# Optimization experiments

Hardware: AMD Instinct MI355X
Metric: run time of the kernel (lower is better)

Reference implementation:

```python
import jax, jax.numpy as jnp
import numpy as np

L, D, F, H = 4, 1024, 2048, 8
DH = D // H
EPS = 1e-5


def setup_inputs() -> dict:
    key = jax.random.key(0)
    ks = jax.random.split(key, 8)
    B, S = 4, 1024
    sd = 1.0 / np.sqrt(D)
    sf = 1.0 / np.sqrt(F)
    return {
        "X": jax.random.normal(ks[0], (B, S, D), jnp.float32),
        "Wq": jax.random.normal(ks[1], (L, D, D), jnp.float32) * sd,
        "Wk": jax.random.normal(ks[2], (L, D, D), jnp.float32) * sd,
        "Wv": jax.random.normal(ks[3], (L, D, D), jnp.float32) * sd,
        "Wg": jax.random.normal(ks[4], (L, D, D), jnp.float32) * sd,
        "Wo": jax.random.normal(ks[5], (L, D, D), jnp.float32) * sd,
        "W1": jax.random.normal(ks[6], (L, D, F), jnp.float32) * sd,
        "W2": jax.random.normal(ks[7], (L, F, D), jnp.float32) * sf,
        "ln_scale": jnp.ones((D,), jnp.float32),
        "ln_bias": jnp.zeros((D,), jnp.float32),
        "gn_scale": jnp.ones((L, D), jnp.float32),
        "gn_bias": jnp.zeros((L, D), jnp.float32),
    }


def _layer_norm(x, scale, bias):
    mu = x.mean(-1, keepdims=True)
    var = x.var(-1, keepdims=True)
    return (x - mu) * jax.lax.rsqrt(var + EPS) * scale + bias


def _rotate(x, cos, sin):
    # x: (B,S,H,DH); cos/sin: (1,S,1,DH//2); rotary pairs (even, odd)
    x1, x2 = x[..., 0::2], x[..., 1::2]
    r1 = x1 * cos - x2 * sin
    r2 = x1 * sin + x2 * cos
    return jnp.stack([r1, r2], axis=-1).reshape(x.shape)


def _decay_matrix(S):
    # D[h,n,m] = gamma_h^(n-m) for n>=m else 0
    gammas = 1.0 - jnp.exp(jnp.linspace(np.log(1 / 32), np.log(1 / 512), H)).astype(jnp.float32)
    n = jnp.arange(S)
    diff = (n[:, None] - n[None, :]).astype(jnp.float32)
    pw = jnp.exp(jnp.clip(diff, 0.0)[None] * jnp.log(gammas)[:, None, None])
    return jnp.where(diff[None] >= 0, pw, 0.0)  # (H,S,S)


def _retention(x, Wq, Wk, Wv, Wg, Wo, gn_s, gn_b, Dm, cos, sin):
    B, S, _ = x.shape
    Q = (x @ Wq).reshape(B, S, H, DH)
    K = (x @ Wk).reshape(B, S, H, DH)
    V = (x @ Wv).reshape(B, S, H, DH)
    Q = _rotate(Q, cos, sin)
    K = _rotate(K, cos, -sin)  # conjugate phase
    att = jnp.einsum('bnhd,bmhd->bhnm', Q, K) * Dm  # (B,H,S,S)
    Y = jnp.einsum('bhnm,bmhd->bnhd', att, V)
    # group norm: normalize each head's output per token
    mu = Y.mean(-1, keepdims=True)
    var = Y.var(-1, keepdims=True)
    Y = (Y - mu) * jax.lax.rsqrt(var + EPS)
    Y = Y.reshape(B, S, D) * gn_s + gn_b
    G = jax.nn.swish(x @ Wg)
    return (G * Y) @ Wo


def reference(X, Wq, Wk, Wv, Wg, Wo, W1, W2, ln_scale, ln_bias, gn_scale, gn_bias):
    B, S, _ = X.shape
    pos = jnp.arange(S, dtype=jnp.float32)
    inv_freq = 1.0 / (10000.0 ** (jnp.arange(0, DH, 2, dtype=jnp.float32) / DH))
    ang = pos[:, None] * inv_freq[None, :]  # (S, DH//2)
    cos = jnp.cos(ang)[None, :, None, :]
    sin = jnp.sin(ang)[None, :, None, :]
    Dm = _decay_matrix(S)
    for i in range(L):
        Yr = _retention(_layer_norm(X, ln_scale, ln_bias), Wq[i], Wk[i], Wv[i],
                        Wg[i], Wo[i], gn_scale[i], gn_bias[i], Dm, cos, sin) + X
        X = jax.nn.gelu(_layer_norm(Yr, ln_scale, ln_bias) @ W1[i]) @ W2[i] + Yr
    return X
```

## Files before the change

### kernel.cpp

```cpp
#include <hip/hip_runtime.h>
#include <hip/hip_bf16.h>
#include <cmath>

#define LAYERS 4
#define Bb 4
#define Ss 1024
#define Dd 1024
#define Ff 2048
#define Hh 8
#define DHd 128
#define Mm (Bb * Ss)
#define EPSf 1e-5f
#define LDQ 4096

typedef __attribute__((ext_vector_type(8))) short short8v;
typedef __attribute__((ext_vector_type(4))) float f32x4;
typedef __attribute__((ext_vector_type(4))) unsigned int u32x4;

__device__ __forceinline__ float swish_f(float x) { return x / (1.f + expf(-x)); }
__device__ __forceinline__ float gelu_f(float x) {
  return 0.5f * x * (1.f + tanhf(0.7978845608028654f * (x + 0.044715f * x * x * x)));
}
__device__ __forceinline__ unsigned short f2bfu(float f) {
  __hip_bfloat16 h = __float2bfloat16(f);
  return __builtin_bit_cast(unsigned short, h);
}
__device__ __forceinline__ float bfu2f(unsigned short u) {
  unsigned v = ((unsigned)u) << 16;
  return __builtin_bit_cast(float, v);
}
__device__ __forceinline__ void gl_lds16(const void* g, void* l) {
  __builtin_amdgcn_global_load_lds((__attribute__((address_space(1))) void*)g,
                                   (__attribute__((address_space(3))) void*)l, 16, 0, 0);
}
__device__ __forceinline__ f32x4 mfma16(short8v a, short8v b, f32x4 c) {
  return __builtin_amdgcn_mfma_f32_16x16x32_bf16(a, b, c, 0, 0, 0);
}

__global__ __launch_bounds__(256) void ln_bf16_kernel(const float* __restrict__ x,
                                                      short* __restrict__ outb,
                                                      const float* __restrict__ sc,
                                                      const float* __restrict__ bi) {
  const int row = blockIdx.x;
  const int t = threadIdx.x;
  const float4 v = *(const float4*)(x + (size_t)row * Dd + t * 4);
  float s = v.x + v.y + v.z + v.w;
  float s2 = v.x * v.x + v.y * v.y + v.z * v.z + v.w * v.w;
#pragma unroll
  for (int o = 32; o > 0; o >>= 1) { s += __shfl_down(s, o); s2 += __shfl_down(s2, o); }
  __shared__ float ps[4], ps2[4];
  if ((t & 63) == 0) { ps[t >> 6] = s; ps2[t >> 6] = s2; }
  __syncthreads();
  s = ps[0] + ps[1] + ps[2] + ps[3];
  s2 = ps2[0] + ps2[1] + ps2[2] + ps2[3];
  const float mu = s * (1.f / Dd);
  const float var = s2 * (1.f / Dd) - mu * mu;
  const float rstd = rsqrtf(var + EPSf);
  const float4 g = *(const float4*)(sc + t * 4);
  const float4 b = *(const float4*)(bi + t * 4);
  const float o0 = (v.x - mu) * rstd * g.x + b.x;
  const float o1 = (v.y - mu) * rstd * g.y + b.y;
  const float o2 = (v.z - mu) * rstd * g.z + b.z;
  const float o3 = (v.w - mu) * rstd * g.w + b.w;
  unsigned p0 = (unsigned)f2bfu(o0) | ((unsigned)f2bfu(o1) << 16);
  unsigned p1 = (unsigned)f2bfu(o2) | ((unsigned)f2bfu(o3) << 16);
  uint2 pk; pk.x = p0; pk.y = p1;
  *(uint2*)(outb + (size_t)row * Dd + t * 4) = pk;
}

__global__ void rope_table_kernel(float* __restrict__ ct, float* __restrict__ st) {
  const int i = blockIdx.x * 256 + threadIdx.x;
  const int s = i >> 6, f = i & 63;
  const float inv = powf(10000.f, -(float)f / 64.f);
  const float a = (float)s * inv;
  ct[i] = cosf(a);
  st[i] = sinf(a);
}

__global__ void rope_ip_kernel(short* __restrict__ QK, const float* __restrict__ ct,
                               const float* __restrict__ st) {
  const int idx = blockIdx.x * 256 + threadIdx.x;
  const int f = idx & 63;
  const int h = (idx >> 6) & 7;
  const int r = idx >> 9;
  const int s = r & (Ss - 1);
  const float c = ct[(s << 6) + f], sn = st[(s << 6) + f];
  const size_t qo = (size_t)r * LDQ + h * DHd + 2 * f;
  const unsigned qp = *(const unsigned*)(QK + qo);
  const unsigned kp = *(const unsigned*)(QK + qo + 1024);
  const float qx = bfu2f((unsigned short)(qp & 0xffff)), qy = bfu2f((unsigned short)(qp >> 16));
  const float kx = bfu2f((unsigned short)(kp & 0xffff)), ky = bfu2f((unsigned short)(kp >> 16));
  const unsigned qn = (unsigned)f2bfu(qx * c - qy * sn) | ((unsigned)f2bfu(qx * sn + qy * c) << 16);
  const unsigned kn = (unsigned)f2bfu(kx * c + ky * sn) | ((unsigned)f2bfu(-kx * sn + ky * c) << 16);
  *(unsigned*)(QK + qo) = qn;
  *(unsigned*)(QK + qo + 1024) = kn;
}

__global__ __launch_bounds__(256) void wtrans4_kernel(const float* __restrict__ W0,
                                                      const float* __restrict__ W1,
                                                      const float* __restrict__ W2,
                                                      const float* __restrict__ W3,
                                                      short* __restrict__ Wt) {
  __shared__ float tile[32][33];
  const int t = threadIdx.x;
  const int n0 = blockIdx.x * 32, k0 = blockIdx.y * 32;
  const int which = n0 >> 10;
  const float* W = (which == 0) ? W0 : (which == 1) ? W1 : (which == 2) ? W2 : W3;
  const int nl = n0 & 1023;
  const int tc = t & 31, tr8 = t >> 5;
#pragma unroll
  for (int i = 0; i < 4; ++i) {
    const int r = tr8 + i * 8;
    tile[r][tc] = W[(size_t)(k0 + r) * 1024 + nl + tc];
  }
  __syncthreads();
#pragma unroll
  for (int i = 0; i < 4; ++i) {
    const int r = tr8 + i * 8;
    Wt[(size_t)(n0 + r) * 1024 + k0 + tc] = (short)f2bfu(tile[tc][r]);
  }
}

__global__ __launch_bounds__(256) void wtrans1_kernel(const float* __restrict__ W,
                                                      short* __restrict__ Wt, int K, int N) {
  __shared__ float tile[32][33];
  const int t = threadIdx.x;
  const int n0 = blockIdx.x * 32, k0 = blockIdx.y * 32;
  const int tc = t & 31, tr8 = t >> 5;
#pragma unroll
  for (int i = 0; i < 4; ++i) {
    const int r = tr8 + i * 8;
    tile[r][tc] = W[(size_t)(k0 + r) * N + n0 + tc];
  }
  __syncthreads();
#pragma unroll
  for (int i = 0; i < 4; ++i) {
    const int r = tr8 + i * 8;
    Wt[(size_t)(n0 + r) * K + k0 + tc] = (short)f2bfu(tile[tc][r]);
  }
}

__global__ __launch_bounds__(256) void vtrans16_kernel(const short* __restrict__ Vb,
                                                       short* __restrict__ Vt) {
  __shared__ short tile[32][33];
  const int t = threadIdx.x;
  const int s0 = blockIdx.x * 32, d0 = blockIdx.y * 32, bh = blockIdx.z;
  const int bb = bh >> 3, h = bh & 7;
  const int tc = t & 31, tr8 = t >> 5;
#pragma unroll
  for (int i = 0; i < 4; ++i) {
    const int r = tr8 + i * 8;
    tile[r][tc] = Vb[(size_t)(bb * Ss + s0 + r) * LDQ + 2048 + h * DHd + d0 + tc];
  }
  __syncthreads();
#pragma unroll
  for (int i = 0; i < 4; ++i) {
    const int r = tr8 + i * 8;
    Vt[(size_t)(bh * DHd + d0 + r) * Ss + s0 + tc] = tile[tc][r];
  }
}

template <int EPI>
__global__ __launch_bounds__(512, 2) void gemm10(const short* __restrict__ A,
                                                 const short* __restrict__ Bt,
                                                 float* __restrict__ Cf,
                                                 short* __restrict__ Cb,
                                                 const float* __restrict__ Res,
                                                 int N, int K, int ldc) {
  __shared__ __align__(16) short As[2][2][128 * 64];
  __shared__ __align__(16) short Bs[2][2][128 * 64];
  const int t = threadIdx.x;
  const int w = t >> 6, l = t & 63;
  const int lq = l >> 4, lr = l & 15;
  const int wr = w >> 2, wc = w & 3;
  const int bhalf = wc >> 1, brow0 = (wc & 1) * 64;
  const int nwg = gridDim.x * gridDim.y;
  const int bid0 = blockIdx.x + blockIdx.y * gridDim.x;
  const int lgid = (bid0 & 7) * (nwg >> 3) + (bid0 >> 3);
  const int bx = lgid % gridDim.x, by = lgid / gridDim.x;
  const int row0 = by * 256, col0 = bx * 256;
  const int NT = K >> 6;

  f32x4 acc[8][4] = {};
  short8v a[4][2], b[4][2];

  auto stageA = [&](int kt, int hf) {
    const int db = kt & 1;
#pragma unroll
    for (int i = 0; i < 2; ++i) {
      const int c = t + i * 512;
      const int row = c >> 3, slot = c & 7;
      gl_lds16(A + (size_t)(row0 + hf * 128 + row) * K + kt * 64 + ((slot ^ (row & 7)) << 3),
               &As[db][hf][c * 8]);
    }
  };
  auto stageB = [&](int kt, int hf) {
    const int db = kt & 1;
#pragma unroll
    for (int i = 0; i < 2; ++i) {
      const int c = t + i * 512;
      const int row = c >> 3, slot = c & 7;
      gl_lds16(Bt + (size_t)(col0 + hf * 128 + row) * K + kt * 64 + ((slot ^ (row & 7)) << 3),
               &Bs[db][hf][c * 8]);
    }
  };
  auto rdA = [&](int db, int m, int ks) -> short8v {
    const int row = m * 16 + lr;
    return *(const short8v*)&As[db][wr][row * 64 + (((ks << 2) + lq) ^ (row & 7)) * 8];
  };
  auto rdB = [&](int db, int n, int ks) -> short8v {
    const int row = brow0 + n * 16 + lr;
    return *(const short8v*)&Bs[db][bhalf][row * 64 + (((ks << 2) + lq) ^ (row & 7)) * 8];
  };

  stageA(0, 0); stageA(0, 1); stageB(0, 0); stageB(0, 1);
  if (NT > 1) { stageB(1, 0); stageB(1, 1); }
  if (NT > 1) { asm volatile("s_waitcnt vmcnt(4)" ::: "memory"); }
  else        { asm volatile("s_waitcnt vmcnt(0)" ::: "memory"); }
  asm volatile("s_barrier" ::: "memory");

  for (int kt = 0; kt < NT; ++kt) {
    const int db = kt & 1;
#pragma unroll
    for (int m = 0; m < 4; ++m) { a[m][0] = rdA(db, m, 0); a[m][1] = rdA(db, m, 1); }
#pragma unroll
    for (int n = 0; n < 2; ++n) { b[n][0] = rdB(db, n, 0); b[n][1] = rdB(db, n, 1); }
    if (kt + 1 < NT) stageA(kt + 1, 0);
    __builtin_amdgcn_s_setprio(1);
#pragma unroll
    for (int m = 0; m < 4; ++m)
#pragma unroll
      for (int n = 0; n < 2; ++n) {
        acc[m][n] = mfma16(a[m][0], b[n][0], acc[m][n]);
        acc[m][n] = mfma16(a[m][1], b[n][1], acc[m][n]);
      }
    __builtin_amdgcn_s_setprio(0);
    asm volatile("s_barrier" ::: "memory");
#pragma unroll
    for (int n = 2; n < 4; ++n) { b[n][0] = rdB(db, n, 0); b[n][1] = rdB(db, n, 1); }
    if (kt + 1 < NT) stageA(kt + 1, 1);
    __builtin_amdgcn_s_setprio(1);
#pragma unroll
    for (int m = 0; m < 4; ++m)
#pragma unroll
      for (int n = 2; n < 4; ++n) {
        acc[m][n] = mfma16(a[m][0], b[n][0], acc[m][n]);
        acc[m][n] = mfma16(a[m][1], b[n][1], acc[m][n]);
      }
    __builtin_amdgcn_s_setprio(0);
    asm volatile("s_barrier" ::: "memory");
#pragma unroll
    for (int m = 0; m < 4; ++m) { a[m][0] = rdA(db, m + 4, 0); a[m][1] = rdA(db, m + 4, 1); }
    if (kt + 2 < NT) stageB(kt + 2, 0);
    __builtin_amdgcn_s_setprio(1);
#pragma unroll
    for (int m = 0; m < 4; ++m)
#pragma unroll
      for (int n = 0; n < 2; ++n) {
        acc[m + 4][n] = mfma16(a[m][0], b[n][0], acc[m + 4][n]);
        acc[m + 4][n] = mfma16(a[m][1], b[n][1], acc[m + 4][n]);
      }
    __builtin_amdgcn_s_setprio(0);
    asm volatile("s_barrier" ::: "memory");
    if (kt + 2 < NT) stageB(kt + 2, 1);
    __builtin_amdgcn_s_setprio(1);
#pragma unroll
    for (int m = 0; m < 4; ++m)
#pragma unroll
      for (int n = 2; n < 4; ++n) {
        acc[m + 4][n] = mfma16(a[m][0], b[n][0], acc[m + 4][n]);
        acc[m + 4][n] = mfma16(a[m][1], b[n][1], acc[m + 4][n]);
      }
    __builtin_amdgcn_s_setprio(0);
    if (kt + 2 < NT) { asm volatile("s_waitcnt vmcnt(4)" ::: "memory"); }
    else             { asm volatile("s_waitcnt vmcnt(0)" ::: "memory"); }
    asm volatile("s_barrier" ::: "memory");
  }

#pragma unroll
  for (int m = 0; m < 8; ++m) {
#pragma unroll
    for (int n = 0; n < 4; ++n) {
#pragma unroll
      for (int r = 0; r < 4; ++r) {
        const int row = row0 + wr * 128 + m * 16 + lq * 4 + r;
        const int col = col0 + wc * 64 + n * 16 + lr;
        const size_t o = (size_t)row * ldc + col;
        float v = acc[m][n][r];
        if (EPI == 0) Cb[o] = (short)f2bfu(v);
        else if (EPI == 1) Cf[o] = v + Res[o];
        else Cb[o] = (short)f2bfu(gelu_f(v));
      }
    }
  }
}

template <int EPI>
__global__ __launch_bounds__(512) void gemm11(const short* __restrict__ A,
                                              const short* __restrict__ Bt,
                                              float* __restrict__ Cf,
                                              short* __restrict__ Cb,
                                              const float* __restrict__ Res,
                                              int K, int lda, int ldb, int ldc, int nxt) {
  __shared__ __align__(16) short As[3][256 * 64];
  __shared__ __align__(16) short Bs[3][128 * 64];
  const int t = threadIdx.x;
  const int w = t >> 6, l = t & 63;
  const int lq = l >> 4, lr = l & 15;
  const int wr = w >> 2, wc = w & 3;
  const int nwg = gridDim.x;
  const int lgid = (blockIdx.x & 7) * (nwg >> 3) + (blockIdx.x >> 3);
  const int mt = lgid / nxt, nt_ = lgid % nxt;
  const int row0 = mt * 256, col0 = nt_ * 128;
  const int NT = K >> 6;
  f32x4 acc[8][2] = {};
  short8v a[4][2], b[2][2];

  auto stageA = [&](int kt, int hf) {
    const int s = kt % 3;
#pragma unroll
    for (int i = 0; i < 2; ++i) {
      const int c = t + i * 512;
      const int row = c >> 3, slot = c & 7;
      gl_lds16(A + (size_t)(row0 + hf * 128 + row) * lda + kt * 64 + ((slot ^ (row & 7)) << 3),
               &As[s][hf * 8192 + c * 8]);
    }
  };
  auto stageB = [&](int kt) {
    const int s = kt % 3;
#pragma unroll
    for (int i = 0; i < 2; ++i) {
      const int c = t + i * 512;
      const int row = c >> 3, slot = c & 7;
      gl_lds16(Bt + (size_t)(col0 + row) * ldb + kt * 64 + ((slot ^ (row & 7)) << 3),
               &Bs[s][c * 8]);
    }
  };
  auto rdA = [&](int s, int m, int ks) -> short8v {
    const int row = wr * 128 + m * 16 + lr;
    return *(const short8v*)&As[s][row * 64 + (((ks << 2) + lq) ^ (row & 7)) * 8];
  };
  auto rdB = [&](int s, int n, int ks) -> short8v {
    const int row = wc * 32 + n * 16 + lr;
    return *(const short8v*)&Bs[s][row * 64 + (((ks << 2) + lq) ^ (row & 7)) * 8];
  };

  stageA(0, 0); stageA(0, 1); stageB(0);
  stageA(1, 0); stageA(1, 1); stageB(1);
  asm volatile("s_waitcnt vmcnt(6)" ::: "memory");
  asm volatile("s_barrier" ::: "memory");

  for (int kt = 0; kt < NT; ++kt) {
    const int s = kt % 3;
#pragma unroll
    for (int m = 0; m < 4; ++m) { a[m][0] = rdA(s, m, 0); a[m][1] = rdA(s, m, 1); }
#pragma unroll
    for (int n = 0; n < 2; ++n) { b[n][0] = rdB(s, n, 0); b[n][1] = rdB(s, n, 1); }
    if (kt + 2 < NT) stageA(kt + 2, 0);
    __builtin_amdgcn_s_setprio(1);
#pragma unroll
    for (int m = 0; m < 4; ++m)
#pragma unroll
      for (int n = 0; n < 2; ++n) {
        acc[m][n] = mfma16(a[m][0], b[n][0], acc[m][n]);
        acc[m][n] = mfma16(a[m][1], b[n][1], acc[m][n]);
      }
    __builtin_amdgcn_s_setprio(0);
    asm volatile("s_barrier" ::: "memory");
#pragma unroll
    for (int m = 0; m < 4; ++m) { a[m][0] = rdA(s, m + 4, 0); a[m][1] = rdA(s, m + 4, 1); }
    if (kt + 2 < NT) { stageA(kt + 2, 1); stageB(kt + 2); }
    __builtin_amdgcn_s_setprio(1);
#pragma unroll
    for (int m = 0; m < 4; ++m)
#pragma unroll
      for (int n = 0; n < 2; ++n) {
        acc[m + 4][n] = mfma16(a[m][0], b[n][0], acc[m + 4][n]);
        acc[m + 4][n] = mfma16(a[m][1], b[n][1], acc[m + 4][n]);
      }
    __builtin_amdgcn_s_setprio(0);
    if (kt + 2 < NT) { asm volatile("s_waitcnt vmcnt(6)" ::: "memory"); }
    else             { asm volatile("s_waitcnt vmcnt(0)" ::: "memory"); }
    asm volatile("s_barrier" ::: "memory");
  }

#pragma unroll
  for (int m = 0; m < 8; ++m) {
#pragma unroll
    for (int n = 0; n < 2; ++n) {
#pragma unroll
      for (int r = 0; r < 4; ++r) {
        const int row = row0 + wr * 128 + m * 16 + lq * 4 + r;
        const int col = col0 + wc * 32 + n * 16 + lr;
        const size_t o = (size_t)row * ldc + col;
        float v = acc[m][n][r];
        if (EPI == 0) Cb[o] = (short)f2bfu(v);
        else if (EPI == 1) Cf[o] = v + Res[o];
        else Cb[o] = (short)f2bfu(gelu_f(v));
      }
    }
  }
}

template <int BM, int BN, int EPI>
__global__ __launch_bounds__(256) void gemm7(const short* __restrict__ A,
                                             const short* __restrict__ Bt,
                                             float* __restrict__ Cf,
                                             short* __restrict__ Cb,
                                             const float* __restrict__ Res,
                                             int N, int K, int ldc) {
  constexpr int NTHR = 256;
  constexpr int WM = BM / 2, WN = BN / 2;
  constexpr int MR = WM / 16, NR = WN / 16;
  constexpr int LA = (BM * 4) / NTHR, LB = (BN * 4) / NTHR;
  __shared__ __align__(16) short As[2][BM * 32];
  __shared__ __align__(16) short Bs[2][BN * 32];
  const int t = threadIdx.x;
  const int w = t >> 6, l = t & 63;
  const int lq = l >> 4, lr = l & 15;
  const int wr = w >> 1, wc = w & 1;
  const int nwg = gridDim.x * gridDim.y;
  const int bid0 = blockIdx.x + blockIdx.y * gridDim.x;
  const int lgid = (bid0 & 7) * (nwg >> 3) + (bid0 >> 3);
  const int bx = lgid % gridDim.x, by = lgid / gridDim.x;
  const int row0 = by * BM, col0 = bx * BN;
  f32x4 acc[MR][NR] = {};
  const int NTK = K >> 5;

  auto stage = [&](int tile, int buf) {
    const int k0 = tile << 5;
#pragma unroll
    for (int i = 0; i < LA; ++i) {
      const int c = t + i * NTHR;
      const int row = c >> 2, sc = c & 3;
      gl_lds16(A + (size_t)(row0 + row) * K + k0 + ((sc ^ ((row >> 1) & 3)) << 3),
               &As[buf][c * 8]);
    }
#pragma unroll
    for (int i = 0; i < LB; ++i) {
      const int c = t + i * NTHR;
      const int row = c >> 2, sc = c & 3;
      gl_lds16(Bt + (size_t)(col0 + row) * K + k0 + ((sc ^ ((row >> 1) & 3)) << 3),
               &Bs[buf][c * 8]);
    }
  };

  stage(0, 0);
  int cur = 0;
  for (int tt = 0; tt < NTK; ++tt) {
    __syncthreads();
    if (tt + 1 < NTK) stage(tt + 1, cur ^ 1);
    short8v a[MR], b[NR];
#pragma unroll
    for (int m = 0; m < MR; ++m) {
      const int row = wr * WM + m * 16 + lr;
      a[m] = *(const short8v*)&As[cur][row * 32 + ((lq ^ ((row >> 1) & 3)) << 3)];
    }
#pragma unroll
    for (int n = 0; n < NR; ++n) {
      const int col = wc * WN + n * 16 + lr;
      b[n] = *(const short8v*)&Bs[cur][col * 32 + ((lq ^ ((col >> 1) & 3)) << 3)];
    }
    __builtin_amdgcn_s_setprio(1);
#pragma unroll
    for (int m = 0; m < MR; ++m)
#pragma unroll
      for (int n = 0; n < NR; ++n) acc[m][n] = mfma16(a[m], b[n], acc[m][n]);
    __builtin_amdgcn_s_setprio(0);
    cur ^= 1;
  }

#pragma unroll
  for (int m = 0; m < MR; ++m) {
#pragma unroll
    for (int n = 0; n < NR; ++n) {
#pragma unroll
      for (int r = 0; r < 4; ++r) {
        const int row = row0 + wr * WM + m * 16 + lq * 4 + r;
        const int col = col0 + wc * WN + n * 16 + lr;
        const size_t o = (size_t)row * ldc + col;
        float v = acc[m][n][r];
        if (EPI == 0) Cb[o] = (short)f2bfu(v);
        else if (EPI == 1) Cf[o] = v + Res[o];
        else Cb[o] = (short)f2bfu(gelu_f(v));
      }
    }
  }
}

__global__ __launch_bounds__(256) void ret4_kernel(const short* __restrict__ QKb,
                                                   const short* __restrict__ Vt,
                                                   float* __restrict__ Y0,
                                                   float* __restrict__ Y1) {
  __shared__ __align__(16) short Ks[2][64 * 128];
  __shared__ __align__(16) short Vs[2][128 * 64];
  const int t = threadIdx.x, w = t >> 6, l = t & 63;
  const int lq = l >> 4, lr = l & 15;
  const int u = blockIdx.x;
  const int lgid = (u & 7) * 64 + (u >> 3);
  const int half = lgid >> 8;
  const int rest = lgid & 255;
  const int bh = rest >> 3, j = rest & 7;
  const int qb = half ? j : 7 - j;
  const int b = bh >> 3, h = bh & 7;
  const int q0 = qb * 128;
  const float lstep = (logf(1.f / 512.f) - logf(1.f / 32.f)) * (1.f / 7.f);
  const float gamma = 1.f - expf(logf(1.f / 32.f) + (float)h * lstep);
  const float l2g = logf(gamma) * 1.44269504f;
  const short* Qp = QKb;
  const short* Kp = QKb + 1024;

  short8v qf[2][4];
#pragma unroll
  for (int qn = 0; qn < 2; ++qn)
#pragma unroll
    for (int ks = 0; ks < 4; ++ks)
      qf[qn][ks] = *(const short8v*)(Qp + (size_t)(b * Ss + q0 + w * 32 + qn * 16 + lr) * LDQ +
                                     h * DHd + ks * 32 + lq * 8);

  float cmf[4], csr[4];
#pragma unroll
  for (int mf = 0; mf < 4; ++mf) cmf[mf] = exp2f(l2g * (float)(-16 * mf));
#pragma unroll
  for (int r = 0; r < 4; ++r) csr[r] = exp2f(l2g * (float)(63 - 4 * lq - r));

  f32x4 yacc[2][8] = {};
  const int nt = 2 * qb + 2;
  const int sb = ((lq & 1) * 2) * 16 + lr;

  auto stageKV = [&](int m0, int buf) {
#pragma unroll
    for (int i = 0; i < 4; ++i) {
      const int c = (w * 4 + i) * 64 + l;
      const int row = c >> 4, slot = c & 15;
      gl_lds16(Kp + (size_t)(b * Ss + m0 + row) * LDQ + h * DHd + ((slot ^ (row & 7)) * 8),
               &Ks[buf][(w * 4 + i) * 512]);
    }
#pragma unroll
    for (int i = 0; i < 4; ++i) {
      const int c = (w * 4 + i) * 64 + l;
      const int row = c >> 3, slot = c & 7;
      gl_lds16(Vt + (size_t)(bh * DHd + row) * Ss + m0 + ((slot ^ (row & 7)) * 8),
               &Vs[buf][(w * 4 + i) * 512]);
    }
  };

  stageKV(half * 64, 0);
  __syncthreads();
  int cur = 0;
  for (int tt = half; tt < nt; tt += 2) {
    const int m0 = tt * 64;
    if (tt + 2 < nt) stageKV((tt + 2) * 64, cur ^ 1);

    f32x4 st[4][2] = {};
    __builtin_amdgcn_s_setprio(1);
#pragma unroll
    for (int mf = 0; mf < 4; ++mf) {
      const int row = mf * 16 + lr;
#pragma unroll
      for (int ks = 0; ks < 4; ++ks) {
        short8v kf = *(const short8v*)&Ks[cur][row * 128 + (((4 * ks + lq) ^ (row & 7)) * 8)];
        st[mf][0] = mfma16(kf, qf[0][ks], st[mf][0]);
        st[mf][1] = mfma16(kf, qf[1][ks], st[mf][1]);
      }
    }
    __builtin_amdgcn_s_setprio(0);
    float rs[2];
#pragma unroll
    for (int qn = 0; qn < 2; ++qn)
      rs[qn] = exp2f(l2g * (float)(q0 + w * 32 + qn * 16 + lr - m0 - 63));
#pragma unroll
    for (int mf = 0; mf < 4; ++mf)
#pragma unroll
      for (int qn = 0; qn < 2; ++qn)
#pragma unroll
        for (int r = 0; r < 4; ++r) {
          const int qg = q0 + w * 32 + qn * 16 + lr;
          const int kvg = m0 + mf * 16 + lq * 4 + r;
          const float wgt = (qg >= kvg) ? rs[qn] * cmf[mf] * csr[r] : 0.f;
          st[mf][qn][r] *= wgt;
        }
    unsigned pk[4][2][2];
#pragma unroll
    for (int mf = 0; mf < 4; ++mf)
#pragma unroll
      for (int qn = 0; qn < 2; ++qn)
#pragma unroll
        for (int p = 0; p < 2; ++p)
          pk[mf][qn][p] = (unsigned)f2bfu(st[mf][qn][2 * p]) |
                          ((unsigned)f2bfu(st[mf][qn][2 * p + 1]) << 16);
    short8v afr[2][2];
#pragma unroll
    for (int qn = 0; qn < 2; ++qn)
#pragma unroll
      for (int ks2 = 0; ks2 < 2; ++ks2) {
        u32x4 wd;
#pragma unroll
        for (int wj = 0; wj < 4; ++wj) {
          const int src = sb + (wj >> 1) * 16;
          const unsigned v0 = __shfl(pk[2 * ks2 + 0][qn][wj & 1], src);
          const unsigned v1 = __shfl(pk[2 * ks2 + 1][qn][wj & 1], src);
          wd[wj] = (lq >= 2) ? v1 : v0;
        }
        afr[qn][ks2] = __builtin_bit_cast(short8v, wd);
      }
    __builtin_amdgcn_s_setprio(1);
#pragma unroll
    for (int nd = 0; nd < 8; ++nd) {
      const int row = nd * 16 + lr;
#pragma unroll
      for (int ks2 = 0; ks2 < 2; ++ks2) {
        short8v vf = *(const short8v*)&Vs[cur][row * 64 + (((4 * ks2 + lq) ^ (row & 7)) * 8)];
        yacc[0][nd] = mfma16(afr[0][ks2], vf, yacc[0][nd]);
        yacc[1][nd] = mfma16(afr[1][ks2], vf, yacc[1][nd]);
      }
    }
    __builtin_amdgcn_s_setprio(0);
    __syncthreads();
    cur ^= 1;
  }
  float* Y = half ? Y1 : Y0;
#pragma unroll
  for (int qn = 0; qn < 2; ++qn)
#pragma unroll
    for (int r = 0; r < 4; ++r) {
      const int q = q0 + w * 32 + qn * 16 + lq * 4 + r;
#pragma unroll
      for (int nd = 0; nd < 8; ++nd)
        Y[(size_t)(b * Ss + q) * Dd + h * DHd + nd * 16 + lr] = yacc[qn][nd][r];
    }
}

__global__ __launch_bounds__(256) void gate_kernel(const float* __restrict__ Y0,
                                                   const float* __restrict__ Y1,
                                                   const short* __restrict__ Graw,
                                                   short* __restrict__ Gb,
                                                   const float* __restrict__ gs,
                                                   const float* __restrict__ gb) {
  const int lane = threadIdx.x & 63;
  const int rowh = blockIdx.x * 4 + (threadIdx.x >> 6);
  const int h = rowh & 7;
  const int row = rowh >> 3;
  const size_t ybase = (size_t)row * Dd + (size_t)h * DHd + lane * 2;
  float2 a = *(const float2*)(Y0 + ybase);
  const float2 c = *(const float2*)(Y1 + ybase);
  a.x += c.x; a.y += c.y;
  float s = a.x + a.y, s2 = a.x * a.x + a.y * a.y;
#pragma unroll
  for (int o = 32; o > 0; o >>= 1) { s += __shfl_down(s, o); s2 += __shfl_down(s2, o); }
  s = __shfl(s, 0);
  s2 = __shfl(s2, 0);
  const float mu = s * (1.f / DHd);
  const float rstd = rsqrtf(s2 * (1.f / DHd) - mu * mu + EPSf);
  const int d = h * DHd + lane * 2;
  const float2 g = *(const float2*)(gs + d);
  const float2 bbv = *(const float2*)(gb + d);
  const float y0 = (a.x - mu) * rstd * g.x + bbv.x;
  const float y1 = (a.y - mu) * rstd * g.y + bbv.y;
  const unsigned gr = *(const unsigned*)(Graw + (size_t)row * LDQ + 3072 + h * DHd + lane * 2);
  const float gx = bfu2f((unsigned short)(gr & 0xffff));
  const float gy = bfu2f((unsigned short)(gr >> 16));
  const unsigned o01 = (unsigned)f2bfu(swish_f(gx) * y0) |
                       ((unsigned)f2bfu(swish_f(gy) * y1) << 16);
  *(unsigned*)(Gb + ybase) = o01;
}

extern "C" void kernel_launch(void* const* d_in, const int* in_sizes, int n_in,
                              void* d_out, int out_size, void* d_ws, size_t ws_size,
                              hipStream_t stream) {
  const float* X = (const float*)d_in[0];
  const float* Wq = (const float*)d_in[1];
  const float* Wk = (const float*)d_in[2];
  const float* Wv = (const float*)d_in[3];
  const float* Wg = (const float*)d_in[4];
  const float* Wo = (const float*)d_in[5];
  const float* W1 = (const float*)d_in[6];
  const float* W2 = (const float*)d_in[7];
  const float* lns = (const float*)d_in[8];
  const float* lnb = (const float*)d_in[9];
  const float* gns = (const float*)d_in[10];
  const float* gnb = (const float*)d_in[11];
  float* out = (float*)d_out;

  char* W = (char*)d_ws;
  const size_t MB = 1u << 20;
  float* Abuf  = (float*)(W);
  short* Xnb   = (short*)(W + 16 * MB);
  short* QKVGb = (short*)(W + 24 * MB);
  float* Y0    = (float*)(W + 56 * MB);
  float* Y1    = (float*)(W + 72 * MB);
  short* Vtb   = (short*)(W + 88 * MB);
  short* Gb    = (short*)(W + 96 * MB);
  short* Wqkvgt= (short*)(W + 104 * MB);
  short* Wot   = (short*)(W + 112 * MB);
  short* W1t   = (short*)(W + 114 * MB);
  short* W2t   = (short*)(W + 118 * MB);
  float* ct    = (float*)(W + 122 * MB);
  float* st    = ct + Ss * 64;
  short* Hb = QKVGb;

  hipMemcpyAsync(Abuf, X, (size_t)Mm * Dd * sizeof(float), hipMemcpyDeviceToDevice, stream);
  rope_table_kernel<<<(Ss * 64) / 256, 256, 0, stream>>>(ct, st);

  for (int l = 0; l < LAYERS; ++l) {
    const size_t DD = (size_t)Dd * Dd;
    wtrans4_kernel<<<dim3(128, 32), 256, 0, stream>>>(Wq + l * DD, Wk + l * DD, Wv + l * DD,
                                                      Wg + l * DD, Wqkvgt);
    wtrans1_kernel<<<dim3(32, 32), 256, 0, stream>>>(Wo + l * DD, Wot, Dd, Dd);
    wtrans1_kernel<<<dim3(64, 32), 256, 0, stream>>>(W1 + (size_t)l * Dd * Ff, W1t, Dd, Ff);
    wtrans1_kernel<<<dim3(32, 64), 256, 0, stream>>>(W2 + (size_t)l * Ff * Dd, W2t, Ff, Dd);

    ln_bf16_kernel<<<Mm, 256, 0, stream>>>(Abuf, Xnb, lns, lnb);
    gemm10<0><<<dim3(16, 16), 512, 0, stream>>>(Xnb, Wqkvgt, nullptr, QKVGb,
                                                nullptr, 4096, Dd, LDQ);
    rope_ip_kernel<<<(Bb * Ss * Hh * 64) / 256, 256, 0, stream>>>(QKVGb, ct, st);
    vtrans16_kernel<<<dim3(Ss / 32, DHd / 32, Bb * Hh), 256, 0, stream>>>(QKVGb, Vtb);
    ret4_kernel<<<512, 256, 0, stream>>>(QKVGb, Vtb, Y0, Y1);
    gate_kernel<<<(Mm * Hh) / 4, 256, 0, stream>>>(Y0, Y1, QKVGb, Gb,
                                                   gns + (size_t)l * Dd, gnb + (size_t)l * Dd);
    gemm7<128, 64, 1><<<dim3(16, 32), 256, 0, stream>>>(Gb, Wot, Abuf, nullptr, Abuf,
                                                        Dd, Dd, Dd);
    ln_bf16_kernel<<<Mm, 256, 0, stream>>>(Abuf, Xnb, lns, lnb);
    gemm11<2><<<256, 512, 0, stream>>>(Xnb, W1t, nullptr, Hb, nullptr,
                                       Dd, Dd, Dd, Ff, 16);
    float* dst = (l == LAYERS - 1) ? out : Abuf;
    gemm7<64, 64, 1><<<dim3(16, 64), 256, 0, stream>>>(Hb, W2t, dst, nullptr, Abuf,
                                                       Dd, Ff, Dd);
  }
}
```

Baseline: 801.2 us.

## Replace gemm7 with triple-buffered 128x128 gemm12 for Wo and W2 projections

Replaces the double-buffered gemm7, which used 32-wide K tiles and 128x64 or 64x64 output tiles, with a new 512-thread gemm12 kernel. gemm12 uses 128x128 tiles, 64-wide K tiles and a three-stage LDS ring with explicit vmcnt waits and barriers. A and B loads are split around the two halves of the MFMA work so copies overlap compute. The aim is more reuse per block and fewer barriers per K step. The Wo and W2 launches drop to 256 workgroups, which lowers occupancy and may leave CUs idle or underused.

```diff
diff --git a/kernel.cpp b/kernel.cpp
--- a/kernel.cpp
+++ b/kernel.cpp
@@ -402,82 +402,101 @@
   }
 }
 
-template <int BM, int BN, int EPI>
-__global__ __launch_bounds__(256) void gemm7(const short* __restrict__ A,
-                                             const short* __restrict__ Bt,
-                                             float* __restrict__ Cf,
-                                             short* __restrict__ Cb,
-                                             const float* __restrict__ Res,
-                                             int N, int K, int ldc) {
-  constexpr int NTHR = 256;
-  constexpr int WM = BM / 2, WN = BN / 2;
-  constexpr int MR = WM / 16, NR = WN / 16;
-  constexpr int LA = (BM * 4) / NTHR, LB = (BN * 4) / NTHR;
-  __shared__ __align__(16) short As[2][BM * 32];
-  __shared__ __align__(16) short Bs[2][BN * 32];
+template <int EPI>
+__global__ __launch_bounds__(512) void gemm12(const short* __restrict__ A,
+                                              const short* __restrict__ Bt,
+                                              float* __restrict__ Cf,
+                                              short* __restrict__ Cb,
+                                              const float* __restrict__ Res,
+                                              int K, int lda, int ldb, int ldc, int nxt) {
+  __shared__ __align__(16) short As[3][128 * 64];
+  __shared__ __align__(16) short Bs[3][128 * 64];
   const int t = threadIdx.x;
   const int w = t >> 6, l = t & 63;
   const int lq = l >> 4, lr = l & 15;
-  const int wr = w >> 1, wc = w & 1;
-  const int nwg = gridDim.x * gridDim.y;
-  const int bid0 = blockIdx.x + blockIdx.y * gridDim.x;
-  const int lgid = (bid0 & 7) * (nwg >> 3) + (bid0 >> 3);
-  const int bx = lgid % gridDim.x, by = lgid / gridDim.x;
-  const int row0 = by * BM, col0 = bx * BN;
-  f32x4 acc[MR][NR] = {};
-  const int NTK = K >> 5;
-
-  auto stage = [&](int tile, int buf) {
-    const int k0 = tile << 5;
-#pragma unroll
-    for (int i = 0; i < LA; ++i) {
-      const int c = t + i * NTHR;
-      const int row = c >> 2, sc = c & 3;
-      gl_lds16(A + (size_t)(row0 + row) * K + k0 + ((sc ^ ((row >> 1) & 3)) << 3),
-               &As[buf][c * 8]);
-    }
-#pragma unroll
-    for (int i = 0; i < LB; ++i) {
-      const int c = t + i * NTHR;
-      const int row = c >> 2, sc = c & 3;
-      gl_lds16(Bt + (size_t)(col0 + row) * K + k0 + ((sc ^ ((row >> 1) & 3)) << 3),
-               &Bs[buf][c * 8]);
-    }
-  };
-
-  stage(0, 0);
-  int cur = 0;
-  for (int tt = 0; tt < NTK; ++tt) {
-    __syncthreads();
-    if (tt + 1 < NTK) stage(tt + 1, cur ^ 1);
-    short8v a[MR], b[NR];
-#pragma unroll
-    for (int m = 0; m < MR; ++m) {
-      const int row = wr * WM + m * 16 + lr;
-      a[m] = *(const short8v*)&As[cur][row * 32 + ((lq ^ ((row >> 1) & 3)) << 3)];
-    }
-#pragma unroll
-    for (int n = 0; n < NR; ++n) {
-      const int col = wc * WN + n * 16 + lr;
-      b[n] = *(const short8v*)&Bs[cur][col * 32 + ((lq ^ ((col >> 1) & 3)) << 3)];
-    }
-    __builtin_amdgcn_s_setprio(1);
-#pragma unroll
-    for (int m = 0; m < MR; ++m)
-#pragma unroll
-      for (int n = 0; n < NR; ++n) acc[m][n] = mfma16(a[m], b[n], acc[m][n]);
-    __builtin_amdgcn_s_setprio(0);
-    cur ^= 1;
-  }
-
-#pragma unroll
-  for (int m = 0; m < MR; ++m) {
-#pragma unroll
-    for (int n = 0; n < NR; ++n) {
+  const int wr = w >> 2, wc = w & 3;
+  const int nwg = gridDim.x;
+  const int lgid = (blockIdx.x & 7) * (nwg >> 3) + (blockIdx.x >> 3);
+  const int mt = lgid / nxt, nt_ = lgid % nxt;
+  const int row0 = mt * 128, col0 = nt_ * 128;
+  const int NT = K >> 6;
+  f32x4 acc[4][2] = {};
+  short8v a[4][2], b[2][2];
+
+  auto stageA = [&](int kt) {
+    const int s = kt % 3;
+#pragma unroll
+    for (int i = 0; i < 2; ++i) {
+      const int c = t + i * 512;
+      const int row = c >> 3, slot = c & 7;
+      gl_lds16(A + (size_t)(row0 + row) * lda + kt * 64 + ((slot ^ (row & 7)) << 3),
+               &As[s][c * 8]);
+    }
+  };
+  auto stageB = [&](int kt) {
+    const int s = kt % 3;
+#pragma unroll
+    for (int i = 0; i < 2; ++i) {
+      const int c = t + i * 512;
+      const int row = c >> 3, slot = c & 7;
+      gl_lds16(Bt + (size_t)(col0 + row) * ldb + kt * 64 + ((slot ^ (row & 7)) << 3),
+               &Bs[s][c * 8]);
+    }
+  };
+  auto rdA = [&](int s, int m, int ks) -> short8v {
+    const int row = wr * 64 + m * 16 + lr;
+    return *(const short8v*)&As[s][row * 64 + (((ks << 2) + lq) ^ (row & 7)) * 8];
+  };
+  auto rdB = [&](int s, int n, int ks) -> short8v {
+    const int row = wc * 32 + n * 16 + lr;
+    return *(const short8v*)&Bs[s][row * 64 + (((ks << 2) + lq) ^ (row & 7)) * 8];
+  };
+
+  stageA(0); stageB(0);
+  stageA(1); stageB(1);
+  asm volatile("s_waitcnt vmcnt(4)" ::: "memory");
+  asm volatile("s_barrier" ::: "memory");
+
+  for (int kt = 0; kt < NT; ++kt) {
+    const int s = kt % 3;
+#pragma unroll
+    for (int m = 0; m < 4; ++m) { a[m][0] = rdA(s, m, 0); a[m][1] = rdA(s, m, 1); }
+#pragma unroll
+    for (int n = 0; n < 2; ++n) { b[n][0] = rdB(s, n, 0); b[n][1] = rdB(s, n, 1); }
+    if (kt + 2 < NT) stageA(kt + 2);
+    __builtin_amdgcn_s_setprio(1);
+#pragma unroll
+    for (int m = 0; m < 2; ++m)
+#pragma unroll
+      for (int n = 0; n < 2; ++n) {
+        acc[m][n] = mfma16(a[m][0], b[n][0], acc[m][n]);
+        acc[m][n] = mfma16(a[m][1], b[n][1], acc[m][n]);
+      }
+    __builtin_amdgcn_s_setprio(0);
+    asm volatile("s_barrier" ::: "memory");
+    if (kt + 2 < NT) stageB(kt + 2);
+    __builtin_amdgcn_s_setprio(1);
+#pragma unroll
+    for (int m = 2; m < 4; ++m)
+#pragma unroll
+      for (int n = 0; n < 2; ++n) {
+        acc[m][n] = mfma16(a[m][0], b[n][0], acc[m][n]);
+        acc[m][n] = mfma16(a[m][1], b[n][1], acc[m][n]);
+      }
+    __builtin_amdgcn_s_setprio(0);
+    if (kt + 2 < NT) { asm volatile("s_waitcnt vmcnt(4)" ::: "memory"); }
+    else             { asm volatile("s_waitcnt vmcnt(0)" ::: "memory"); }
+    asm volatile("s_barrier" ::: "memory");
+  }
+
+#pragma unroll
+  for (int m = 0; m < 4; ++m) {
+#pragma unroll
+    for (int n = 0; n < 2; ++n) {
 #pragma unroll
       for (int r = 0; r < 4; ++r) {
-        const int row = row0 + wr * WM + m * 16 + lq * 4 + r;
-        const int col = col0 + wc * WN + n * 16 + lr;
+        const int row = row0 + wr * 64 + m * 16 + lq * 4 + r;
+        const int col = col0 + wc * 32 + n * 16 + lr;
         const size_t o = (size_t)row * ldc + col;
         float v = acc[m][n][r];
         if (EPI == 0) Cb[o] = (short)f2bfu(v);
@@ -718,13 +737,13 @@
     ret4_kernel<<<512, 256, 0, stream>>>(QKVGb, Vtb, Y0, Y1);
     gate_kernel<<<(Mm * Hh) / 4, 256, 0, stream>>>(Y0, Y1, QKVGb, Gb,
                                                    gns + (size_t)l * Dd, gnb + (size_t)l * Dd);
-    gemm7<128, 64, 1><<<dim3(16, 32), 256, 0, stream>>>(Gb, Wot, Abuf, nullptr, Abuf,
-                                                        Dd, Dd, Dd);
+    gemm12<1><<<256, 512, 0, stream>>>(Gb, Wot, Abuf, nullptr, Abuf,
+                                       Dd, Dd, Dd, Dd, 8);
     ln_bf16_kernel<<<Mm, 256, 0, stream>>>(Abuf, Xnb, lns, lnb);
     gemm11<2><<<256, 512, 0, stream>>>(Xnb, W1t, nullptr, Hb, nullptr,
                                        Dd, Dd, Dd, Ff, 16);
     float* dst = (l == LAYERS - 1) ? out : Abuf;
-    gemm7<64, 64, 1><<<dim3(16, 64), 256, 0, stream>>>(Hb, W2t, dst, nullptr, Abuf,
-                                                       Dd, Ff, Dd);
-  }
-}
+    gemm12<1><<<256, 512, 0, stream>>>(Hb, W2t, dst, nullptr, Abuf,
+                                       Ff, Ff, Ff, Dd, 8);
+  }
+}
```

New measurement: 767.4 us. 1.04x faster.
